# Performance work log

Measured on AMD Instinct MI355X. Metric: run time of the kernel, lower is better.

## Reference

```python
import jax, jax.numpy as jnp
import numpy as np
import math

N_HEADS = 8
D_EMBED = 512
D_CROSS = 768
D_HEAD = D_EMBED // N_HEADS


def _conv1x1(w, b, t):
    # 1x1 conv == pointwise matmul over channel dim. t: [B, Cin, H, W], w: [Cout, Cin]
    out = jnp.einsum('oc,bchw->bohw', w, t)
    return out + b[None, :, None, None]


def setup_inputs() -> dict:
    key = jax.random.key(0)
    ks = jax.random.split(key, 10)
    s = 0.02
    return {
        'x': jax.random.normal(ks[0], (8, D_EMBED, 32, 32), dtype=jnp.float32),
        'y': jax.random.normal(ks[1], (8, D_CROSS, 32, 32), dtype=jnp.float32),
        'w_q': jax.random.normal(ks[2], (D_EMBED, D_EMBED), dtype=jnp.float32) * s,
        'b_q': jnp.zeros((D_EMBED,), dtype=jnp.float32),
        'w_k': jax.random.normal(ks[3], (D_EMBED, D_CROSS), dtype=jnp.float32) * s,
        'b_k': jnp.zeros((D_EMBED,), dtype=jnp.float32),
        'w_v': jax.random.normal(ks[4], (D_EMBED, D_CROSS), dtype=jnp.float32) * s,
        'b_v': jnp.zeros((D_EMBED,), dtype=jnp.float32),
        'w_o': jax.random.normal(ks[5], (D_EMBED, D_EMBED), dtype=jnp.float32) * s,
        'b_o': jnp.zeros((D_EMBED,), dtype=jnp.float32),
    }


def reference(x, y, w_q, b_q, w_k, b_k, w_v, b_v, w_o, b_o):
    B, C, H, W = x.shape
    N = H * W
    q = _conv1x1(w_q, b_q, x)  # [B, C, H, W]
    k = _conv1x1(w_k, b_k, y)
    v = _conv1x1(w_v, b_v, y)
    # flat reshape [B, C, H, W] -> [B, nH, d_head, N] (row-major, matches torch .view)
    q = q.reshape(B, N_HEADS, D_HEAD, N)
    k = k.reshape(B, N_HEADS, D_HEAD, N)
    v = v.reshape(B, N_HEADS, D_HEAD, N)
    # attn = q^T k / sqrt(d_head): [B, nH, N, N]
    scores = jnp.einsum('bhdq,bhdk->bhqk', q, k) / math.sqrt(D_HEAD)
    attn = jax.nn.softmax(scores, axis=-1)
    # out = attn @ v^T : [B, nH, N, d_head]
    out = jnp.einsum('bhqk,bhdk->bhqd', attn, v)
    # faithful quirk: flat reshape (no transpose back) to [B, C, H, W]
    out = out.reshape(B, N_HEADS * D_HEAD, H, W)
    return _conv1x1(w_o, b_o, out)
```

## Files before the change

### kernel.cpp

```cpp
#include <hip/hip_runtime.h>
#include <cstddef>
#include <cstdint>


typedef short bs8 __attribute__((ext_vector_type(8)));
typedef short bs4 __attribute__((ext_vector_type(4)));
typedef float fx4 __attribute__((ext_vector_type(4)));
typedef unsigned ux4 __attribute__((ext_vector_type(4)));

#define MFMA16(a, b, c) __builtin_amdgcn_mfma_f32_16x16x32_bf16((a), (b), (c), 0, 0, 0)

#define GLOAD_LDS16(g, l)                                                  \
  __builtin_amdgcn_global_load_lds(                                        \
      (const __attribute__((address_space(1))) void*)(g),                  \
      (__attribute__((address_space(3))) void*)(l), 16, 0, 0)

__device__ __forceinline__ short f2b(float f) {
  unsigned u = __builtin_bit_cast(unsigned, f);
  u = (u + 0x7fff + ((u >> 16) & 1)) >> 16;
  return (short)u;
}

__device__ __forceinline__ unsigned cvt_pk_bf16(float lo, float hi) {
  unsigned r;
  asm("v_cvt_pk_bf16_f32 %0, %1, %2" : "=v"(r) : "v"(lo), "v"(hi));
  return r;
}

__device__ __forceinline__ float exp2_fast(float x) {
  float r;
  asm("v_exp_f32 %0, %1" : "=v"(r) : "v"(x));
  return r;
}

#define QSCALE 0.1803368801111244f

__global__ __launch_bounds__(256) void prep(
    const float* __restrict__ w_q, const float* __restrict__ w_k,
    const float* __restrict__ w_v, const float* __restrict__ w_o,
    short* __restrict__ wdst,
    const float* __restrict__ x, short* __restrict__ xt,
    const float* __restrict__ y, short* __restrict__ yt)
{
  __shared__ short T[64][72];
  const int bid = blockIdx.x;
  const int t = threadIdx.x;

  if (bid < 1280) {
    const int i = bid * 1024 + t * 4;
    const float* src; int off;
    if (i < 262144)       { src = w_q; off = 0; }
    else if (i < 655360)  { src = w_k; off = 262144; }
    else if (i < 1048576) { src = w_v; off = 655360; }
    else                  { src = w_o; off = 1048576; }
    float4 f = *(const float4*)(src + (i - off));
    bs4 o; o[0] = f2b(f.x); o[1] = f2b(f.y); o[2] = f2b(f.z); o[3] = f2b(f.w);
    *(bs4*)(wdst + i) = o;
    return;
  }

  const float* src; short* dst; int C, nt, ct, b;
  if (bid < 2304) {
    const int local = bid - 1280;
    src = x; dst = xt; C = 512;
    nt = local & 15; ct = (local >> 4) & 7; b = local >> 7;
  } else {
    const int local = bid - 2304;
    src = y; dst = yt; C = 768;
    nt = local & 15; const int rest = local >> 4; ct = rest % 12; b = rest / 12;
  }

  const size_t srcBase = ((size_t)b * C + ct * 64) * 1024 + nt * 64;
  #pragma unroll
  for (int p = 0; p < 4; ++p) {
    const int lin = p * 256 + t;
    const int row = lin >> 4;
    const int seg = lin & 15;
    float4 f = *(const float4*)(src + srcBase + (size_t)row * 1024 + seg * 4);
    T[seg * 4 + 0][row] = f2b(f.x);
    T[seg * 4 + 1][row] = f2b(f.y);
    T[seg * 4 + 2][row] = f2b(f.z);
    T[seg * 4 + 3][row] = f2b(f.w);
  }
  __syncthreads();
  const size_t dstBase = ((size_t)b * 1024 + nt * 64) * C + ct * 64;
  #pragma unroll
  for (int p = 0; p < 2; ++p) {
    const int lin = p * 256 + t;
    const int row = lin >> 3;
    const int seg = lin & 7;
    *(bs8*)(dst + dstBase + (size_t)row * C + seg * 8) = *(const bs8*)&T[row][seg * 8];
  }
}

template<int MODE, int MTL2>
__device__ __forceinline__ void gemm2_body(
    short* As0, short* As1, short* Bs0, short* Bs1, int hw, int tid,
    const short* __restrict__ W, const short* __restrict__ Xt,
    const float* __restrict__ bias, const float* __restrict__ bias2,
    void* __restrict__ Cout, void* __restrict__ Cout2, int K, float scale)
{
  const int wid = tid >> 6, l = tid & 63;
  const int swz = (hw & 7) * (8 << MTL2) + (hw >> 3);
  const int n0 = (swz & 7) * 128;
  const int m0 = ((swz >> 3) & ((1 << MTL2) - 1)) * 128;
  const int b  = swz >> (3 + MTL2);
  const int wm = wid >> 2, wn = wid & 3;

  const int lrow = l >> 3;
  const int swz8 = ((l & 7) ^ lrow) * 8;
  const int x7 = l & 7;

  const short* Wg = W + (size_t)m0 * K;
  const short* Xg = Xt + ((size_t)b * 1024 + n0) * K;

  fx4 acc[4][2] = {};
  const int NK = K >> 6;

  #pragma unroll
  for (int j = 0; j < 2; ++j) {
    const int rb = j * 64 + wid * 8;
    const int row = rb + lrow;
    GLOAD_LDS16(Wg + (size_t)row * K + swz8, As0 + rb * 64);
    GLOAD_LDS16(Xg + (size_t)row * K + swz8, Bs0 + rb * 64);
  }
  __syncthreads();

  auto gstep = [&](const short* AsC, const short* BsC, short* AsN, short* BsN,
                   int kn, bool pre) {
    if (pre) {
      #pragma unroll
      for (int j = 0; j < 2; ++j) {
        const int rb = j * 64 + wid * 8;
        const int row = rb + lrow;
        GLOAD_LDS16(Wg + (size_t)row * K + kn + swz8, AsN + rb * 64);
        GLOAD_LDS16(Xg + (size_t)row * K + kn + swz8, BsN + rb * 64);
      }
    }
    #pragma unroll
    for (int kb = 0; kb < 2; ++kb) {
      bs8 af[4], bfr[2];
      const int u = (kb * 4 + (l >> 4)) ^ x7;
      #pragma unroll
      for (int ms = 0; ms < 4; ++ms) {
        const int rr = wm * 64 + ms * 16 + (l & 15);
        af[ms] = *(const bs8*)&AsC[rr * 64 + u * 8];
      }
      #pragma unroll
      for (int ns = 0; ns < 2; ++ns) {
        const int rr = wn * 32 + ns * 16 + (l & 15);
        bfr[ns] = *(const bs8*)&BsC[rr * 64 + u * 8];
      }
      #pragma unroll
      for (int ms = 0; ms < 4; ++ms)
        #pragma unroll
        for (int ns = 0; ns < 2; ++ns)
          acc[ms][ns] = MFMA16(af[ms], bfr[ns], acc[ms][ns]);
    }
    __syncthreads();
  };

  const int NK2 = NK >> 1;
  for (int p = 0; p < NK2; ++p) {
    gstep(As0, Bs0, As1, Bs1, (2 * p + 1) * 64, true);
    gstep(As1, Bs1, As0, Bs0, (2 * p + 2) * 64, (2 * p + 2) < NK);
  }

  #pragma unroll
  for (int ms = 0; ms < 4; ++ms) {
    #pragma unroll
    for (int ns = 0; ns < 2; ++ns) {
      const int n = n0 + wn * 32 + ns * 16 + (l & 15);
      const int mb = m0 + wm * 64 + ms * 16 + (l >> 4) * 4;
      if (MODE == 0) {
        const float f0 = (acc[ms][ns][0] + bias[mb + 0]) * scale;
        const float f1 = (acc[ms][ns][1] + bias[mb + 1]) * scale;
        const float f2 = (acc[ms][ns][2] + bias[mb + 2]) * scale;
        const float f3 = (acc[ms][ns][3] + bias[mb + 3]) * scale;
        uint2 od; od.x = cvt_pk_bf16(f0, f1); od.y = cvt_pk_bf16(f2, f3);
        short* dst = (short*)Cout + (((size_t)b * 8 + (mb >> 6)) * 1024 + n) * 64 + (mb & 63);
        *(uint2*)dst = od;
      } else if (MODE == 2) {
        #pragma unroll
        for (int r = 0; r < 4; ++r)
          ((float*)Cout)[((size_t)b * 512 + mb + r) * 1024 + n] = acc[ms][ns][r] + bias[mb + r];
      } else {
        if (mb < 512) {
          const float f0 = acc[ms][ns][0] + bias[mb + 0];
          const float f1 = acc[ms][ns][1] + bias[mb + 1];
          const float f2 = acc[ms][ns][2] + bias[mb + 2];
          const float f3 = acc[ms][ns][3] + bias[mb + 3];
          uint2 od; od.x = cvt_pk_bf16(f0, f1); od.y = cvt_pk_bf16(f2, f3);
          short* dst = (short*)Cout + (((size_t)b * 8 + (mb >> 6)) * 1024 + n) * 64 + (mb & 63);
          *(uint2*)dst = od;
        } else {
          const int c = mb - 512;
          #pragma unroll
          for (int r = 0; r < 4; ++r)
            ((short*)Cout2)[((size_t)b * 512 + c + r) * 1024 + n] = f2b(acc[ms][ns][r] + bias2[c + r]);
        }
      }
    }
  }
}

__global__ __launch_bounds__(512) void gemm_qkv(
    const short* __restrict__ wq, const short* __restrict__ wkv,
    const short* __restrict__ xt, const short* __restrict__ yt,
    const float* __restrict__ b_q, const float* __restrict__ b_k,
    const float* __restrict__ b_v,
    short* __restrict__ Qw, short* __restrict__ Kw, short* __restrict__ Vw)
{
  __shared__ short As[2][128 * 64];
  __shared__ short Bs[2][128 * 64];
  if (blockIdx.x < 256)
    gemm2_body<0, 2>(As[0], As[1], Bs[0], Bs[1], blockIdx.x, threadIdx.x,
                     wq, xt, b_q, nullptr, (void*)Qw, nullptr, 512, QSCALE);
  else
    gemm2_body<3, 3>(As[0], As[1], Bs[0], Bs[1], blockIdx.x - 256, threadIdx.x,
                     wkv, yt, b_k, b_v, (void*)Kw, (void*)Vw, 768, 1.0f);
}

__global__ __launch_bounds__(512) void gemm_o(
    const short* __restrict__ wo, const short* __restrict__ Ot,
    const float* __restrict__ b_o, float* __restrict__ out)
{
  __shared__ short As[2][128 * 64];
  __shared__ short Bs[2][128 * 64];
  gemm2_body<2, 2>(As[0], As[1], Bs[0], Bs[1], blockIdx.x, threadIdx.x,
                   wo, Ot, b_o, nullptr, (void*)out, nullptr, 512, 1.0f);
}

__global__ __launch_bounds__(512) void attn_mfma(
    const short* __restrict__ Q, const short* __restrict__ Kt,
    const short* __restrict__ V, short* __restrict__ Ot)
{
  __shared__ short Ks[2][64 * 64];
  __shared__ short Vs[2][64 * 64];
  __shared__ short Ps[8][16 * 64];

  const int t = threadIdx.x, wid = t >> 6, l = t & 63;
  const int hw = blockIdx.x;
  const int swzb = (hw & 7) * 64 + (hw >> 3);
  const int qt = swzb & 7, h = (swzb >> 3) & 7, b = swzb >> 6;
  const int q0 = qt * 128 + wid * 16;
  const size_t bh = (size_t)b * 8 + h;

  const short* Qg = Q + (bh * 1024 + q0) * 64;
  const short* Kg = Kt + bh * 1024 * 64;
  const short* Vg = V + bh * 64 * 1024;

  const int g = l >> 4;
  const int q = l & 15;
  const int x7 = q & 7;
  const int lrow = l >> 3;
  const int swz8 = ((l & 7) ^ lrow) * 8;
  short* Pw = Ps[wid];

  const bs8 onesf = {0x3F80, 0x3F80, 0x3F80, 0x3F80,
                     0x3F80, 0x3F80, 0x3F80, 0x3F80};

  bs8 qf[2];
  #pragma unroll
  for (int db = 0; db < 2; ++db)
    qf[db] = *(const bs8*)(Qg + (size_t)q * 64 + db * 32 + g * 8);

  {
    const int row = wid * 8 + lrow;
    GLOAD_LDS16(Kg + (size_t)row * 64 + swz8, &Ks[0][wid * 8 * 64]);
    GLOAD_LDS16(Vg + (size_t)row * 1024 + swz8, &Vs[0][wid * 8 * 64]);
  }
  __syncthreads();

  fx4 oacc[4] = {};
  fx4 lacc = {};

  auto tile = [&](const short* KsC, const short* VsC, short* KsN, short* VsN,
                  int ktn, bool pre) {
    if (pre) {
      const int k0n = ktn * 64;
      const int row = wid * 8 + lrow;
      GLOAD_LDS16(Kg + (size_t)(k0n + row) * 64 + swz8, KsN + wid * 8 * 64);
      GLOAD_LDS16(Vg + (size_t)row * 1024 + k0n + swz8, VsN + wid * 8 * 64);
    }

    fx4 s[4] = {};
    __builtin_amdgcn_s_setprio(1);
    #pragma unroll
    for (int ks = 0; ks < 4; ++ks) {
      const int rr = ks * 16 + q;
      #pragma unroll
      for (int db = 0; db < 2; ++db) {
        bs8 kf = *(const bs8*)&KsC[rr * 64 + ((db * 4 + g) ^ x7) * 8];
        s[ks] = MFMA16(kf, qf[db], s[ks]);
      }
    }
    __builtin_amdgcn_s_setprio(0);

    #pragma unroll
    for (int ks = 0; ks < 4; ++ks)
      #pragma unroll
      for (int r = 0; r < 4; ++r)
        s[ks][r] = exp2_fast(s[ks][r]);

    #pragma unroll
    for (int ks = 0; ks < 4; ++ks) {
      uint2 pd;
      pd.x = cvt_pk_bf16(s[ks][0], s[ks][1]);
      pd.y = cvt_pk_bf16(s[ks][2], s[ks][3]);
      const int u16 = ks * 2 + (g >> 1);
      *(uint2*)&Pw[q * 64 + (u16 ^ x7) * 8 + (g & 1) * 4] = pd;
    }

    __builtin_amdgcn_s_setprio(1);
    #pragma unroll
    for (int kb = 0; kb < 2; ++kb) {
      const int u = kb * 4 + g;
      bs8 pf = *(const bs8*)&Pw[q * 64 + (u ^ x7) * 8];
      lacc = MFMA16(pf, onesf, lacc);
      #pragma unroll
      for (int ds = 0; ds < 4; ++ds) {
        const int d = ds * 16 + q;
        bs8 vf = *(const bs8*)&VsC[d * 64 + (u ^ x7) * 8];
        oacc[ds] = MFMA16(pf, vf, oacc[ds]);
      }
    }
    __builtin_amdgcn_s_setprio(0);
    __syncthreads();
  };

  #pragma unroll 1
  for (int p = 0; p < 8; ++p) {
    tile(Ks[0], Vs[0], Ks[1], Vs[1], 2 * p + 1, true);
    tile(Ks[1], Vs[1], Ks[0], Vs[0], 2 * p + 2, p < 7);
  }

  __syncthreads();
  short* Sq = &Ps[0][0];
  float linv[4];
  #pragma unroll
  for (int r = 0; r < 4; ++r) linv[r] = 1.f / lacc[r];
  #pragma unroll
  for (int ds = 0; ds < 4; ++ds) {
    const int d = ds * 16 + q;
    #pragma unroll
    for (int r = 0; r < 4; ++r) {
      const int tok = (g * 4 + r) * 64 + d;
      Sq[tok * 8 + wid] = f2b(oacc[ds][r] * linv[r]);
    }
  }
  __syncthreads();
  short* OtB = Ot + ((size_t)b * 1024) * 512 + h * 64 + qt * 8;
  #pragma unroll
  for (int rr = 0; rr < 2; ++rr) {
    const int tok = rr * 512 + t;
    *(ux4*)(OtB + (size_t)tok * 512) = *(const ux4*)&Sq[tok * 8];
  }
}

extern "C" void kernel_launch(void* const* d_in, const int* in_sizes, int n_in,
                              void* d_out, int out_size, void* d_ws, size_t ws_size,
                              hipStream_t stream) {
  const float* x   = (const float*)d_in[0];
  const float* y   = (const float*)d_in[1];
  const float* w_q = (const float*)d_in[2];
  const float* b_q = (const float*)d_in[3];
  const float* w_k = (const float*)d_in[4];
  const float* b_k = (const float*)d_in[5];
  const float* w_v = (const float*)d_in[6];
  const float* b_v = (const float*)d_in[7];
  const float* w_o = (const float*)d_in[8];
  const float* b_o = (const float*)d_in[9];

  char* ws = (char*)d_ws;
  const size_t MiB = 1u << 20;
  short* xt  = (short*)(ws);
  short* yt  = (short*)(ws + 8 * MiB);
  short* Qw  = (short*)(ws + 20 * MiB);
  short* Kw  = (short*)(ws + 28 * MiB);
  short* Vw  = (short*)(ws + 36 * MiB);
  short* Ot  = (short*)(ws + 52 * MiB);
  short* wqb = (short*)(ws + 60 * MiB);
  short* wkb = wqb + 262144;
  short* wob = wkb + 786432;

  hipLaunchKernelGGL(prep, dim3(3840), dim3(256), 0, stream,
                     w_q, w_k, w_v, w_o, wqb, x, xt, y, yt);
  hipLaunchKernelGGL(gemm_qkv, dim3(768), dim3(512), 0, stream,
                     wqb, wkb, xt, yt, b_q, b_k, b_v, Qw, Kw, Vw);
  hipLaunchKernelGGL(attn_mfma, dim3(512), dim3(512), 0, stream, Qw, Kw, Vw, Ot);
  hipLaunchKernelGGL(gemm_o, dim3(256), dim3(512), 0, stream, wob, Ot, b_o, (float*)d_out);
}
```

Before: 75.86 us.

## Use 4-wave single-buffered 64x64 warp tiles for QKV projection GEMM

```diff
diff --git a/kernel.cpp b/kernel.cpp
--- a/kernel.cpp
+++ b/kernel.cpp
@@ -93,6 +93,109 @@
   }
 }
 
+template<int MODE>
+__device__ __forceinline__ void gemm_store(
+    fx4 a, int b, int mb, int n,
+    const float* __restrict__ bias, const float* __restrict__ bias2,
+    void* __restrict__ Cout, void* __restrict__ Cout2, float scale)
+{
+  if (MODE == 0) {
+    const float f0 = (a[0] + bias[mb + 0]) * scale;
+    const float f1 = (a[1] + bias[mb + 1]) * scale;
+    const float f2 = (a[2] + bias[mb + 2]) * scale;
+    const float f3 = (a[3] + bias[mb + 3]) * scale;
+    uint2 od; od.x = cvt_pk_bf16(f0, f1); od.y = cvt_pk_bf16(f2, f3);
+    short* dst = (short*)Cout + (((size_t)b * 8 + (mb >> 6)) * 1024 + n) * 64 + (mb & 63);
+    *(uint2*)dst = od;
+  } else if (MODE == 2) {
+    #pragma unroll
+    for (int r = 0; r < 4; ++r)
+      ((float*)Cout)[((size_t)b * 512 + mb + r) * 1024 + n] = a[r] + bias[mb + r];
+  } else {
+    if (mb < 512) {
+      const float f0 = a[0] + bias[mb + 0];
+      const float f1 = a[1] + bias[mb + 1];
+      const float f2 = a[2] + bias[mb + 2];
+      const float f3 = a[3] + bias[mb + 3];
+      uint2 od; od.x = cvt_pk_bf16(f0, f1); od.y = cvt_pk_bf16(f2, f3);
+      short* dst = (short*)Cout + (((size_t)b * 8 + (mb >> 6)) * 1024 + n) * 64 + (mb & 63);
+      *(uint2*)dst = od;
+    } else {
+      const int c = mb - 512;
+      #pragma unroll
+      for (int r = 0; r < 4; ++r)
+        ((short*)Cout2)[((size_t)b * 512 + c + r) * 1024 + n] = f2b(a[r] + bias2[c + r]);
+    }
+  }
+}
+
+template<int MODE, int MTL2>
+__device__ __forceinline__ void gemm3_body(
+    short* As, short* Bs, int hw, int tid,
+    const short* __restrict__ W, const short* __restrict__ Xt,
+    const float* __restrict__ bias, const float* __restrict__ bias2,
+    void* __restrict__ Cout, void* __restrict__ Cout2, int K, float scale)
+{
+  const int wid = tid >> 6, l = tid & 63;
+  const int swz = (hw & 7) * (8 << MTL2) + (hw >> 3);
+  const int n0 = (swz & 7) * 128;
+  const int m0 = ((swz >> 3) & ((1 << MTL2) - 1)) * 128;
+  const int b  = swz >> (3 + MTL2);
+  const int wm = wid >> 1, wn = wid & 1;
+
+  const int lrow = l >> 3;
+  const int swz8 = ((l & 7) ^ lrow) * 8;
+  const int x7 = l & 7;
+
+  const short* Wg = W + (size_t)m0 * K;
+  const short* Xg = Xt + ((size_t)b * 1024 + n0) * K;
+
+  fx4 acc[4][4] = {};
+  const int NK = K >> 6;
+
+  for (int kt = 0; kt < NK; ++kt) {
+    if (kt) __syncthreads();
+    const int k0 = kt * 64;
+    #pragma unroll
+    for (int j = 0; j < 4; ++j) {
+      const int rb = j * 32 + wid * 8;
+      const int row = rb + lrow;
+      GLOAD_LDS16(Wg + (size_t)row * K + k0 + swz8, As + rb * 64);
+      GLOAD_LDS16(Xg + (size_t)row * K + k0 + swz8, Bs + rb * 64);
+    }
+    __syncthreads();
+    #pragma unroll
+    for (int kb = 0; kb < 2; ++kb) {
+      bs8 af[4], bfr[4];
+      const int u = (kb * 4 + (l >> 4)) ^ x7;
+      #pragma unroll
+      for (int ms = 0; ms < 4; ++ms) {
+        const int rr = wm * 64 + ms * 16 + (l & 15);
+        af[ms] = *(const bs8*)&As[rr * 64 + u * 8];
+      }
+      #pragma unroll
+      for (int ns = 0; ns < 4; ++ns) {
+        const int rr = wn * 64 + ns * 16 + (l & 15);
+        bfr[ns] = *(const bs8*)&Bs[rr * 64 + u * 8];
+      }
+      #pragma unroll
+      for (int ms = 0; ms < 4; ++ms)
+        #pragma unroll
+        for (int ns = 0; ns < 4; ++ns)
+          acc[ms][ns] = MFMA16(af[ms], bfr[ns], acc[ms][ns]);
+    }
+  }
+
+  #pragma unroll
+  for (int ms = 0; ms < 4; ++ms)
+    #pragma unroll
+    for (int ns = 0; ns < 4; ++ns) {
+      const int n = n0 + wn * 64 + ns * 16 + (l & 15);
+      const int mb = m0 + wm * 64 + ms * 16 + (l >> 4) * 4;
+      gemm_store<MODE>(acc[ms][ns], b, mb, n, bias, bias2, Cout, Cout2, scale);
+    }
+}
+
 template<int MODE, int MTL2>
 __device__ __forceinline__ void gemm2_body(
     short* As0, short* As1, short* Bs0, short* Bs1, int hw, int tid,
@@ -167,57 +270,29 @@
   }
 
   #pragma unroll
-  for (int ms = 0; ms < 4; ++ms) {
+  for (int ms = 0; ms < 4; ++ms)
     #pragma unroll
     for (int ns = 0; ns < 2; ++ns) {
       const int n = n0 + wn * 32 + ns * 16 + (l & 15);
       const int mb = m0 + wm * 64 + ms * 16 + (l >> 4) * 4;
-      if (MODE == 0) {
-        const float f0 = (acc[ms][ns][0] + bias[mb + 0]) * scale;
-        const float f1 = (acc[ms][ns][1] + bias[mb + 1]) * scale;
-        const float f2 = (acc[ms][ns][2] + bias[mb + 2]) * scale;
-        const float f3 = (acc[ms][ns][3] + bias[mb + 3]) * scale;
-        uint2 od; od.x = cvt_pk_bf16(f0, f1); od.y = cvt_pk_bf16(f2, f3);
-        short* dst = (short*)Cout + (((size_t)b * 8 + (mb >> 6)) * 1024 + n) * 64 + (mb & 63);
-        *(uint2*)dst = od;
-      } else if (MODE == 2) {
-        #pragma unroll
-        for (int r = 0; r < 4; ++r)
-          ((float*)Cout)[((size_t)b * 512 + mb + r) * 1024 + n] = acc[ms][ns][r] + bias[mb + r];
-      } else {
-        if (mb < 512) {
-          const float f0 = acc[ms][ns][0] + bias[mb + 0];
-          const float f1 = acc[ms][ns][1] + bias[mb + 1];
-          const float f2 = acc[ms][ns][2] + bias[mb + 2];
-          const float f3 = acc[ms][ns][3] + bias[mb + 3];
-          uint2 od; od.x = cvt_pk_bf16(f0, f1); od.y = cvt_pk_bf16(f2, f3);
-          short* dst = (short*)Cout + (((size_t)b * 8 + (mb >> 6)) * 1024 + n) * 64 + (mb & 63);
-          *(uint2*)dst = od;
-        } else {
-          const int c = mb - 512;
-          #pragma unroll
-          for (int r = 0; r < 4; ++r)
-            ((short*)Cout2)[((size_t)b * 512 + c + r) * 1024 + n] = f2b(acc[ms][ns][r] + bias2[c + r]);
-        }
-      }
-    }
-  }
-}
-
-__global__ __launch_bounds__(512) void gemm_qkv(
+      gemm_store<MODE>(acc[ms][ns], b, mb, n, bias, bias2, Cout, Cout2, scale);
+    }
+}
+
+__global__ __launch_bounds__(256) void gemm_qkv(
     const short* __restrict__ wq, const short* __restrict__ wkv,
     const short* __restrict__ xt, const short* __restrict__ yt,
     const float* __restrict__ b_q, const float* __restrict__ b_k,
     const float* __restrict__ b_v,
     short* __restrict__ Qw, short* __restrict__ Kw, short* __restrict__ Vw)
 {
-  __shared__ short As[2][128 * 64];
-  __shared__ short Bs[2][128 * 64];
+  __shared__ short As[128 * 64];
+  __shared__ short Bs[128 * 64];
   if (blockIdx.x < 256)
-    gemm2_body<0, 2>(As[0], As[1], Bs[0], Bs[1], blockIdx.x, threadIdx.x,
+    gemm3_body<0, 2>(As, Bs, blockIdx.x, threadIdx.x,
                      wq, xt, b_q, nullptr, (void*)Qw, nullptr, 512, QSCALE);
   else
-    gemm2_body<3, 3>(As[0], As[1], Bs[0], Bs[1], blockIdx.x - 256, threadIdx.x,
+    gemm3_body<3, 3>(As, Bs, blockIdx.x - 256, threadIdx.x,
                      wkv, yt, b_k, b_v, (void*)Kw, (void*)Vw, 768, 1.0f);
 }
 
@@ -386,7 +461,7 @@
 
   hipLaunchKernelGGL(prep, dim3(3840), dim3(256), 0, stream,
                      w_q, w_k, w_v, w_o, wqb, x, xt, y, yt);
-  hipLaunchKernelGGL(gemm_qkv, dim3(768), dim3(512), 0, stream,
+  hipLaunchKernelGGL(gemm_qkv, dim3(768), dim3(256), 0, stream,
                      wqb, wkb, xt, yt, b_q, b_k, b_v, Qw, Kw, Vw);
   hipLaunchKernelGGL(attn_mfma, dim3(512), dim3(512), 0, stream, Qw, Kw, Vw, Ot);
   hipLaunchKernelGGL(gemm_o, dim3(256), dim3(512), 0, stream, wob, Ot, b_o, (float*)d_out);
```

Result: no change. 76.14 us (+0.4%).

## Triple-buffer K/V tiles in attention with two-deep async prefetch

Applied to the files above, without the earlier changes.

```diff
diff --git a/kernel.cpp b/kernel.cpp
--- a/kernel.cpp
+++ b/kernel.cpp
@@ -93,6 +93,42 @@
   }
 }
 
+template<int MODE>
+__device__ __forceinline__ void gemm_store(
+    fx4 a, int b, int mb, int n,
+    const float* __restrict__ bias, const float* __restrict__ bias2,
+    void* __restrict__ Cout, void* __restrict__ Cout2, float scale)
+{
+  if (MODE == 0) {
+    const float f0 = (a[0] + bias[mb + 0]) * scale;
+    const float f1 = (a[1] + bias[mb + 1]) * scale;
+    const float f2 = (a[2] + bias[mb + 2]) * scale;
+    const float f3 = (a[3] + bias[mb + 3]) * scale;
+    uint2 od; od.x = cvt_pk_bf16(f0, f1); od.y = cvt_pk_bf16(f2, f3);
+    short* dst = (short*)Cout + (((size_t)b * 8 + (mb >> 6)) * 1024 + n) * 64 + (mb & 63);
+    *(uint2*)dst = od;
+  } else if (MODE == 2) {
+    #pragma unroll
+    for (int r = 0; r < 4; ++r)
+      ((float*)Cout)[((size_t)b * 512 + mb + r) * 1024 + n] = a[r] + bias[mb + r];
+  } else {
+    if (mb < 512) {
+      const float f0 = a[0] + bias[mb + 0];
+      const float f1 = a[1] + bias[mb + 1];
+      const float f2 = a[2] + bias[mb + 2];
+      const float f3 = a[3] + bias[mb + 3];
+      uint2 od; od.x = cvt_pk_bf16(f0, f1); od.y = cvt_pk_bf16(f2, f3);
+      short* dst = (short*)Cout + (((size_t)b * 8 + (mb >> 6)) * 1024 + n) * 64 + (mb & 63);
+      *(uint2*)dst = od;
+    } else {
+      const int c = mb - 512;
+      #pragma unroll
+      for (int r = 0; r < 4; ++r)
+        ((short*)Cout2)[((size_t)b * 512 + c + r) * 1024 + n] = f2b(a[r] + bias2[c + r]);
+    }
+  }
+}
+
 template<int MODE, int MTL2>
 __device__ __forceinline__ void gemm2_body(
     short* As0, short* As1, short* Bs0, short* Bs1, int hw, int tid,
@@ -167,41 +203,13 @@
   }
 
   #pragma unroll
-  for (int ms = 0; ms < 4; ++ms) {
+  for (int ms = 0; ms < 4; ++ms)
     #pragma unroll
     for (int ns = 0; ns < 2; ++ns) {
       const int n = n0 + wn * 32 + ns * 16 + (l & 15);
       const int mb = m0 + wm * 64 + ms * 16 + (l >> 4) * 4;
-      if (MODE == 0) {
-        const float f0 = (acc[ms][ns][0] + bias[mb + 0]) * scale;
-        const float f1 = (acc[ms][ns][1] + bias[mb + 1]) * scale;
-        const float f2 = (acc[ms][ns][2] + bias[mb + 2]) * scale;
-        const float f3 = (acc[ms][ns][3] + bias[mb + 3]) * scale;
-        uint2 od; od.x = cvt_pk_bf16(f0, f1); od.y = cvt_pk_bf16(f2, f3);
-        short* dst = (short*)Cout + (((size_t)b * 8 + (mb >> 6)) * 1024 + n) * 64 + (mb & 63);
-        *(uint2*)dst = od;
-      } else if (MODE == 2) {
-        #pragma unroll
-        for (int r = 0; r < 4; ++r)
-          ((float*)Cout)[((size_t)b * 512 + mb + r) * 1024 + n] = acc[ms][ns][r] + bias[mb + r];
-      } else {
-        if (mb < 512) {
-          const float f0 = acc[ms][ns][0] + bias[mb + 0];
-          const float f1 = acc[ms][ns][1] + bias[mb + 1];
-          const float f2 = acc[ms][ns][2] + bias[mb + 2];
-          const float f3 = acc[ms][ns][3] + bias[mb + 3];
-          uint2 od; od.x = cvt_pk_bf16(f0, f1); od.y = cvt_pk_bf16(f2, f3);
-          short* dst = (short*)Cout + (((size_t)b * 8 + (mb >> 6)) * 1024 + n) * 64 + (mb & 63);
-          *(uint2*)dst = od;
-        } else {
-          const int c = mb - 512;
-          #pragma unroll
-          for (int r = 0; r < 4; ++r)
-            ((short*)Cout2)[((size_t)b * 512 + c + r) * 1024 + n] = f2b(acc[ms][ns][r] + bias2[c + r]);
-        }
-      }
-    }
-  }
+      gemm_store<MODE>(acc[ms][ns], b, mb, n, bias, bias2, Cout, Cout2, scale);
+    }
 }
 
 __global__ __launch_bounds__(512) void gemm_qkv(
@@ -235,8 +243,8 @@
     const short* __restrict__ Q, const short* __restrict__ Kt,
     const short* __restrict__ V, short* __restrict__ Ot)
 {
-  __shared__ short Ks[2][64 * 64];
-  __shared__ short Vs[2][64 * 64];
+  __shared__ short Ks[3][64 * 64];
+  __shared__ short Vs[3][64 * 64];
   __shared__ short Ps[8][16 * 64];
 
   const int t = threadIdx.x, wid = t >> 6, l = t & 63;
@@ -265,24 +273,27 @@
   for (int db = 0; db < 2; ++db)
     qf[db] = *(const bs8*)(Qg + (size_t)q * 64 + db * 32 + g * 8);
 
-  {
+  auto stage = [&](int kt, int buf) {
     const int row = wid * 8 + lrow;
-    GLOAD_LDS16(Kg + (size_t)row * 64 + swz8, &Ks[0][wid * 8 * 64]);
-    GLOAD_LDS16(Vg + (size_t)row * 1024 + swz8, &Vs[0][wid * 8 * 64]);
-  }
-  __syncthreads();
+    GLOAD_LDS16(Kg + (size_t)(kt * 64 + row) * 64 + swz8, &Ks[buf][wid * 8 * 64]);
+    GLOAD_LDS16(Vg + (size_t)row * 1024 + kt * 64 + swz8, &Vs[buf][wid * 8 * 64]);
+  };
+
+  stage(0, 0);
+  stage(1, 1);
+  asm volatile("s_waitcnt vmcnt(2)\n\ts_barrier" ::: "memory");
 
   fx4 oacc[4] = {};
   fx4 lacc = {};
 
-  auto tile = [&](const short* KsC, const short* VsC, short* KsN, short* VsN,
-                  int ktn, bool pre) {
-    if (pre) {
-      const int k0n = ktn * 64;
-      const int row = wid * 8 + lrow;
-      GLOAD_LDS16(Kg + (size_t)(k0n + row) * 64 + swz8, KsN + wid * 8 * 64);
-      GLOAD_LDS16(Vg + (size_t)row * 1024 + k0n + swz8, VsN + wid * 8 * 64);
-    }
+  int cur = 0;
+  #pragma unroll 1
+  for (int kt = 0; kt < 16; ++kt) {
+    int stg = cur + 2; if (stg >= 3) stg -= 3;
+    if (kt + 2 < 16) stage(kt + 2, stg);
+
+    const short* KsC = Ks[cur];
+    const short* VsC = Vs[cur];
 
     fx4 s[4] = {};
     __builtin_amdgcn_s_setprio(1);
@@ -326,13 +337,13 @@
       }
     }
     __builtin_amdgcn_s_setprio(0);
-    __syncthreads();
-  };
-
-  #pragma unroll 1
-  for (int p = 0; p < 8; ++p) {
-    tile(Ks[0], Vs[0], Ks[1], Vs[1], 2 * p + 1, true);
-    tile(Ks[1], Vs[1], Ks[0], Vs[0], 2 * p + 2, p < 7);
+
+    if (kt < 14)
+      asm volatile("s_waitcnt vmcnt(2)\n\ts_barrier" ::: "memory");
+    else if (kt == 14)
+      asm volatile("s_waitcnt vmcnt(0)\n\ts_barrier" ::: "memory");
+
+    cur = (cur == 2) ? 0 : cur + 1;
   }
 
   __syncthreads();
```

Result: no change. 76.85 us (+1.3%).
